# Kernel tuning notes

Measured on AMD Instinct MI355X. Metric: run time of the kernel, lower is better.

## Reference

```python
import jax, jax.numpy as jnp
import numpy as np

ELU = jax.nn.elu
RELU = jax.nn.relu


def _mlp(x, W0, b0, Wh, bh, Wo, bo, act):
    # first hidden layer, stacked middle hidden layers, linear output layer
    h = act(x @ W0 + b0)
    for i in range(Wh.shape[0]):
        h = act(h @ Wh[i] + bh[i])
    return h @ Wo + bo


def _gru_layer(x_seq, h0, Wi, Wh, bi, bh):
    # torch nn.GRU gate math. x_seq: (T,B,I), h0: (B,H)
    xi = x_seq @ Wi.T + bi  # (T,B,3H) precomputed input projection

    def step(h, xt):
        hh = h @ Wh.T + bh
        xr, xz, xn = jnp.split(xt, 3, -1)
        hr, hz, hn = jnp.split(hh, 3, -1)
        r = jax.nn.sigmoid(xr + hr)
        z = jax.nn.sigmoid(xz + hz)
        n = jnp.tanh(xn + r * hn)
        hnew = (1.0 - z) * n + z * h
        return hnew, hnew

    hT, ys = jax.lax.scan(step, h0, xi)
    return ys, hT


def setup_inputs() -> dict:
    key = jax.random.key(0)
    ks = iter(jax.random.split(key, 64))
    B, T = 1024, 512
    S, SE, OE, GH = 4, 16, 16, 16
    OBJ_N, NULL_N, NOBJ = 3, 4, 7
    p = lambda *shape: jax.random.normal(next(ks), shape, jnp.float32) * 0.1
    return dict(
        envs=jax.random.normal(next(ks), (B, 9), jnp.float32),
        states=jax.random.normal(next(ks), (B, T, S), jnp.float32),
        # state embedder: 4 -> [16]*4 -> 16 (relu)
        se_W0=p(S, SE), se_b0=p(SE), se_Wh=p(3, SE, SE), se_bh=p(3, SE), se_Wo=p(SE, SE), se_bo=p(SE),
        # per-object embedders: 3 -> [16]*4 -> 16 (elu), stacked over 3 objects
        oe_W0=p(OBJ_N, 3, OE), oe_b0=p(OBJ_N, OE), oe_Wh=p(OBJ_N, 3, OE, OE), oe_bh=p(OBJ_N, 3, OE),
        oe_Wo=p(OBJ_N, OE, OE), oe_bo=p(OBJ_N, OE),
        null_embed=jax.random.uniform(next(ks), (NULL_N, OE), jnp.float32),
        init_gru_h=jax.random.uniform(next(ks), (2, GH), jnp.float32),
        # attention-score mlp: 32 -> [16]*3 -> 1 (elu)
        att_W0=p(SE + OE, 16), att_b0=p(16), att_Wh=p(2, 16, 16), att_bh=p(2, 16), att_Wo=p(16, 1), att_bo=p(1),
        # GRU: 2 layers, input 128, hidden 16
        gru0_Wi=p(3 * GH, SE + OE * NOBJ), gru0_Wh=p(3 * GH, GH), gru0_bi=p(3 * GH), gru0_bh=p(3 * GH),
        gru1_Wi=p(3 * GH, GH), gru1_Wh=p(3 * GH, GH), gru1_bi=p(3 * GH), gru1_bh=p(3 * GH),
        # relation MLPs: 32 -> [8]*2 -> 8 (elu), stacked over 7 slots
        rel_W0=p(NOBJ, GH + OE, 8), rel_b0=p(NOBJ, 8), rel_Wh=p(NOBJ, 1, 8, 8), rel_bh=p(NOBJ, 1, 8),
        rel_Wo=p(NOBJ, 8, 8), rel_bo=p(NOBJ, 8),
        # final mlp: 72 -> [4]*2 -> 4 (elu)
        fin_W0=p(GH + 8 * NOBJ, S), fin_b0=p(S), fin_Wh=p(1, S, S), fin_bh=p(1, S), fin_Wo=p(S, S), fin_bo=p(S),
        predict_t=0,
    )


def reference(envs, states, se_W0, se_b0, se_Wh, se_bh, se_Wo, se_bo,
              oe_W0, oe_b0, oe_Wh, oe_bh, oe_Wo, oe_bo,
              null_embed, init_gru_h,
              att_W0, att_b0, att_Wh, att_bh, att_Wo, att_bo,
              gru0_Wi, gru0_Wh, gru0_bi, gru0_bh, gru1_Wi, gru1_Wh, gru1_bi, gru1_bh,
              rel_W0, rel_b0, rel_Wh, rel_bh, rel_Wo, rel_bo,
              fin_W0, fin_b0, fin_Wh, fin_bh, fin_Wo, fin_bo,
              predict_t):
    B = envs.shape[0]
    T = states.shape[1]
    NOBJ = rel_W0.shape[0]  # 7 = obj_n + nullobj_n
    OE = null_embed.shape[1]

    # per-object embeddings: split envs into obj_n chunks, run per-slot MLPs (grouped via vmap)
    env_objs = envs.reshape(B, 3, 3).transpose(1, 0, 2)  # (3,B,3)
    obj_real = jax.vmap(lambda x, W0, b0, Wh, bh, Wo, bo: _mlp(x, W0, b0, Wh, bh, Wo, bo, ELU))(
        env_objs, oe_W0, oe_b0, oe_Wh, oe_bh, oe_Wo, oe_bo)  # (3,B,16)
    obj_null = jnp.broadcast_to(null_embed[:, None, :], (null_embed.shape[0], B, OE))  # (4,B,16)
    obj_embd = jnp.concatenate([obj_real, obj_null], 0)           # (7,B,16)
    obj_t = jnp.broadcast_to(obj_embd[:, None], (NOBJ, T, B, OE))  # (7,T,B,16)

    # state embedding over the full sequence (time-major like torch GRU)
    se = _mlp(states.transpose(1, 0, 2), se_W0, se_b0, se_Wh, se_bh, se_Wo, se_bo, RELU)  # (T,B,16)

    # attention scores per object slot
    def score_fn(emb):
        xin = jnp.concatenate([se, emb], -1)  # (T,B,32)
        return _mlp(xin, att_W0, att_b0, att_Wh, att_bh, att_Wo, att_bo, ELU)[..., 0]
    scores = jax.vmap(score_fn)(obj_t)  # (7,T,B)
    # PermuteLayer reverses the slot ordering before softmax over slots
    col_scores = jax.nn.softmax(jnp.flip(scores, 0), axis=0)  # (7,T,B)

    # GRU over [state_emb ; all obj embeds]
    gru_in = jnp.concatenate([se, jnp.moveaxis(obj_t, 0, 2).reshape(T, B, NOBJ * OE)], -1)  # (T,B,128)
    h0 = jnp.broadcast_to(init_gru_h[:, None, :], (2, B, init_gru_h.shape[1]))
    y0, _ = _gru_layer(gru_in, h0[0], gru0_Wi, gru0_Wh, gru0_bi, gru0_bh)
    gru_out, _ = _gru_layer(y0, h0[1], gru1_Wi, gru1_Wh, gru1_bi, gru1_bh)  # (T,B,16)

    # per-slot relation MLPs weighted by attention
    def rel_fn(emb, w, W0, b0, Wh, bh, Wo, bo):
        xin = jnp.concatenate([gru_out, emb], -1)  # (T,B,32)
        r = _mlp(xin, W0, b0, Wh, bh, Wo, bo, ELU)  # (T,B,8)
        return r * w[..., None]
    weighted = jax.vmap(rel_fn)(obj_t, col_scores, rel_W0, rel_b0, rel_Wh, rel_bh, rel_Wo, rel_bo)  # (7,T,B,8)

    final_in = jnp.concatenate([gru_out, jnp.moveaxis(weighted, 0, 2).reshape(T, B, -1)], -1)  # (T,B,72)
    out = _mlp(final_in, fin_W0, fin_b0, fin_Wh, fin_bh, fin_Wo, fin_bo, ELU)  # (T,B,4)
    return out.transpose(1, 0, 2)  # (B,T,4)
```

## Files before the change

kernel.cpp:

```cpp
#include <hip/hip_runtime.h>
#include <hip/hip_bf16.h>
#include <hip/hip_fp16.h>
#include <stdint.h>

#define TLEN 512
#define TCW 48
#define NCHK 11
__device__ __forceinline__ int csize(int i){ return (i == 10) ? 32 : 48; }

typedef unsigned short u16;
typedef unsigned int u32;

__device__ __forceinline__ float b2f(u16 u){ union{u32 i; float f;} v; v.i = ((u32)u)<<16; return v.f; }
__device__ __forceinline__ u16 f2bf(float f){
    union{float f; u32 i;} v; v.f = f;
    u32 b = v.i; b += 0x7fffu + ((b>>16)&1u);
    return (u16)(b>>16);
}
__device__ __forceinline__ float fexp2(float x){ return __builtin_amdgcn_exp2f(x); }
__device__ __forceinline__ float frcp(float x){ return __builtin_amdgcn_rcpf(x); }
#define LOG2E 1.4426950408889634f
__device__ __forceinline__ float elu_f(float x){ return x > 0.f ? x : fexp2(x*LOG2E) - 1.f; }
__device__ __forceinline__ float sigm(float x){ return frcp(1.f + fexp2(-LOG2E*x)); }
__device__ __forceinline__ float tanh_f(float x){ return 1.f - 2.f*frcp(1.f + fexp2((2.f*LOG2E)*x)); }

__device__ __forceinline__ float ldg(const void* p, int i, bool F){
    return F ? ((const float*)p)[i] : b2f(((const u16*)p)[i]);
}

__device__ void fill(float* dst, const void* src, int n, int tid, int nt, bool F){
    for (int i = tid; i < n; i += nt) dst[i] = ldg(src, i, F);
}
__device__ void fillS(float* dst, const void* src, int R, int C, int stride, int tid, int nt, bool F){
    for (int i = tid; i < R*C; i += nt){ int r = i / C, c = i % C; dst[i] = ldg(src, r*stride + c, F); }
}
__device__ void fillT(float* dst, const void* src, int K, int I, int stride, int tid, int nt, bool F){
    for (int idx = tid; idx < K*I; idx += nt){ int i = idx / K, k = idx % K; dst[idx] = ldg(src, k*stride + i, F); }
}

__global__ __launch_bounds__(256,1) void fused(
    const void* envs, const void* states,
    const void* se_W0, const void* se_b0, const void* se_Wh, const void* se_bh, const void* se_Wo, const void* se_bo,
    const void* oe_W0, const void* oe_b0, const void* oe_Wh, const void* oe_bh, const void* oe_Wo, const void* oe_bo,
    const void* null_embed, const void* init_h,
    const void* att_W0, const void* att_b0, const void* att_Wh, const void* att_bh, const void* att_Wo, const void* att_bo,
    const void* gru0_Wi, const void* gru0_Wh, const void* gru0_bi, const void* gru0_bh,
    const void* gru1_Wi, const void* gru1_Wh, const void* gru1_bi, const void* gru1_bh,
    const void* rel_W0, const void* rel_b0, const void* rel_Wh, const void* rel_bh, const void* rel_Wo, const void* rel_bo,
    const void* fin_W0, const void* fin_b0, const void* fin_Wh, const void* fin_bh, const void* fin_Wo, const void* fin_bo,
    void* out)
{
    __shared__ float sW0T[64], sb0[16], sWhT[768], sbh[48], sWoT[256], sbo[16];
    __shared__ float aW0T[256], aWhT[512], abh[32], aWo[16], abo_s[1];
    __shared__ float wi0se[768];
    __shared__ float rW0T[896], rWhT[448], rbh[56], rWoT[448], rbo[56];
    __shared__ float fW0T[288], fb0[4], fWhT[16], fbh[4], fWoT[16], fbo[4];
    __shared__ float E_att[448], E_rel[224], base_xi[192];
    __shared__ float g0bhn[16], g1bi48[48], g1bh48[48];
    __shared__ float uni[14016];
    __shared__ int s_isf32;

    const int tid = threadIdx.x, nt = 256;
    const int blk = blockIdx.x;
    const int wid = tid >> 6, ln = tid & 63;

    _Float16* bufA = (_Float16*)(uni);
    _Float16* bufB = (_Float16*)(uni + 4608);
    _Float16* gruA = (_Float16*)(uni + 9216);
    _Float16* gruB = (_Float16*)(uni + 10752);
    _Float16* cscA = (_Float16*)(uni + 12288);
    _Float16* cscB = (_Float16*)(uni + 12960);
    float*    invA = uni + 13632;
    float*    invB = uni + 13824;

    if (tid == 0){
        const u16* p = (const u16*)se_W0;
        int ok = 1;
        #pragma unroll
        for (int k = 0; k < 8; k++){
            float v = fabsf(b2f(p[2*k]));
            ok &= (v > 1e-12f && v < 16.f) ? 1 : 0;
        }
        s_isf32 = ok ? 0 : 1;
    }
    __syncthreads();
    const bool F = (s_isf32 != 0);

    fillT(sW0T, se_W0, 4, 16, 16, tid, nt, F);
    fill (sb0, se_b0, 16, tid, nt, F);
    for (int l = 0; l < 3; l++) fillT(sWhT + l*256, (const u16*)se_Wh + (F?l*512:l*256), 16, 16, 16, tid, nt, F);
    fill (sbh, se_bh, 48, tid, nt, F);
    fillT(sWoT, se_Wo, 16, 16, 16, tid, nt, F);
    fill (sbo, se_bo, 16, tid, nt, F);
    fillT(aW0T, att_W0, 16, 16, 16, tid, nt, F);
    for (int l = 0; l < 2; l++) fillT(aWhT + l*256, (const u16*)att_Wh + (F?l*512:l*256), 16, 16, 16, tid, nt, F);
    fill (abh, att_bh, 32, tid, nt, F);
    fill (aWo, att_Wo, 16, tid, nt, F);
    fill (abo_s, att_bo, 1, tid, nt, F);
    fillS(wi0se, gru0_Wi, 48, 16, 128, tid, nt, F);
    for (int s = 0; s < 7; s++){
        fillT(rW0T + s*128, (const u16*)rel_W0 + (F?s*512:s*256), 16, 8, 8, tid, nt, F);
        fillT(rWhT + s*64, (const u16*)rel_Wh + (F?s*128:s*64), 8, 8, 8, tid, nt, F);
        fillT(rWoT + s*64, (const u16*)rel_Wo + (F?s*128:s*64), 8, 8, 8, tid, nt, F);
    }
    fill (rbh, rel_bh, 56, tid, nt, F);
    fill (rbo, rel_bo, 56, tid, nt, F);
    fillT(fW0T, fin_W0, 72, 4, 4, tid, nt, F);
    fill (fb0, fin_b0, 4, tid, nt, F);
    fillT(fWhT, fin_Wh, 4, 4, 4, tid, nt, F);
    fill (fbh, fin_bh, 4, tid, nt, F);
    fillT(fWoT, fin_Wo, 4, 4, 4, tid, nt, F);
    fill (fbo, fin_bo, 4, tid, nt, F);
    fill (g0bhn, (const u16*)gru0_bh + (F?64:32), 16, tid, nt, F);
    fill (g1bi48, gru1_bi, 48, tid, nt, F);
    fill (g1bh48, gru1_bh, 48, tid, nt, F);
    float* oeW0T = uni;
    float* oeb0  = uni + 144;
    float* oeWhT = uni + 192;
    float* oebh  = uni + 2496;
    float* oeWoT = uni + 2640;
    float* oebo  = uni + 3408;
    float* aW0To = uni + 3456;
    float* ab0   = uni + 3712;
    float* rW0To = uni + 3728;
    float* objE  = uni + 4624;
    for (int s = 0; s < 3; s++){
        fillT(oeW0T + s*48, (const u16*)oe_W0 + (F?s*96:s*48), 3, 16, 16, tid, nt, F);
        for (int l = 0; l < 3; l++)
            fillT(oeWhT + (s*3+l)*256, (const u16*)oe_Wh + (F?(s*3+l)*512:(s*3+l)*256), 16, 16, 16, tid, nt, F);
        fillT(oeWoT + s*256, (const u16*)oe_Wo + (F?s*512:s*256), 16, 16, 16, tid, nt, F);
    }
    fill(oeb0, oe_b0, 48, tid, nt, F);
    fill(oebh, oe_bh, 144, tid, nt, F);
    fill(oebo, oe_bo, 48, tid, nt, F);
    fillT(aW0To, (const u16*)att_W0 + (F?512:256), 16, 16, 16, tid, nt, F);
    fill (ab0, att_b0, 16, tid, nt, F);
    for (int s = 0; s < 7; s++)
        fillT(rW0To + s*128, (const u16*)rel_W0 + (F?(s*512+256):(s*256+128)), 16, 8, 8, tid, nt, F);
    __syncthreads();

    if (tid < 28){
        int b1 = tid / 7, s = tid % 7;
        float o[16];
        if (s < 3){
            int b = blk*4 + b1;
            float x0 = ldg(envs, b*9+3*s, F), x1 = ldg(envs, b*9+3*s+1, F), x2 = ldg(envs, b*9+3*s+2, F);
            float h[16], h2[16];
            #pragma unroll
            for (int i = 0; i < 16; i++){
                float a = oeb0[s*16+i] + x0*oeW0T[s*48+i*3] + x1*oeW0T[s*48+i*3+1] + x2*oeW0T[s*48+i*3+2];
                h[i] = elu_f(a);
            }
            for (int l = 0; l < 3; l++){
                #pragma unroll
                for (int i = 0; i < 16; i++){
                    float a = oebh[(s*3+l)*16+i];
                    #pragma unroll
                    for (int k = 0; k < 16; k++) a += h[k]*oeWhT[((s*3+l)*16+i)*16+k];
                    h2[i] = elu_f(a);
                }
                #pragma unroll
                for (int i = 0; i < 16; i++) h[i] = h2[i];
            }
            #pragma unroll
            for (int i = 0; i < 16; i++){
                float a = oebo[s*16+i];
                #pragma unroll
                for (int k = 0; k < 16; k++) a += h[k]*oeWoT[(s*16+i)*16+k];
                o[i] = a;
            }
        } else {
            #pragma unroll
            for (int i = 0; i < 16; i++) o[i] = ldg(null_embed, (s-3)*16 + i, F);
        }
        #pragma unroll
        for (int i = 0; i < 16; i++) objE[(b1*7+s)*16 + i] = o[i];
    }
    __syncthreads();

    for (int idx = tid; idx < 448; idx += nt){
        int r = idx % 112, i = r % 16;
        int os = (idx / 16) * 16;
        float a = ab0[i];
        #pragma unroll
        for (int k = 0; k < 16; k++) a += objE[os + k]*aW0To[i*16+k];
        E_att[idx] = a;
    }
    for (int idx = tid; idx < 224; idx += nt){
        int r = idx % 56, s = r / 8, i = r % 8;
        int b1 = idx / 56;
        float a = ldg(rel_b0, s*8+i, F);
        #pragma unroll
        for (int k = 0; k < 16; k++) a += objE[(b1*7+s)*16 + k]*rW0To[(s*8+i)*16+k];
        E_rel[idx] = a;
    }
    for (int idx = tid; idx < 192; idx += nt){
        int b1 = idx / 48, g = idx % 48;
        float a = ldg(gru0_bi, g, F) + (g < 32 ? ldg(gru0_bh, g, F) : 0.f);
        for (int s = 0; s < 7; s++){
            int wb = g*128 + 16 + s*16;
            #pragma unroll
            for (int k = 0; k < 16; k++) a += objE[(b1*7+s)*16 + k]*ldg(gru0_Wi, wb+k, F);
        }
        base_xi[idx] = a;
    }

    const int lj = ln & 15;
    const int gbase = ln & 48;
    float hp0 = 0.f, hp1 = 0.f;
    if (wid == 0){
        hp0 = ldg(init_h, lj, F);
        hp1 = ldg(init_h, 16 + lj, F);
    }
    const int mtid = tid - 64;
    const int b1p = (wid >= 1) ? (mtid / 48) : 0;
    const int tl  = (wid >= 1) ? (mtid % 48) : 0;
    const int bb  = blk*4 + b1p;
    __syncthreads();

    for (int c = 0; c <= NCHK+1; c++){
        if (wid == 0){
            if (c >= 1 && c <= NCHK){
                const int cs = c-1;
                const int tcs = csize(cs);
                const _Float16* xb = (cs&1) ? bufB : bufA;
                _Float16*       gb = (cs&1) ? gruB : gruA;
                float w0r[16], w0z[16], w0n[16], wi1r[16], wi1z[16], wi1n[16], wh1r[16], wh1z[16], wh1n[16];
                #pragma unroll
                for (int k = 0; k < 16; k++){
                    w0r[k]  = ldg(gru0_Wh, lj*16+k, F);
                    w0z[k]  = ldg(gru0_Wh, (16+lj)*16+k, F);
                    w0n[k]  = ldg(gru0_Wh, (32+lj)*16+k, F);
                    wi1r[k] = ldg(gru1_Wi, lj*16+k, F);
                    wi1z[k] = ldg(gru1_Wi, (16+lj)*16+k, F);
                    wi1n[k] = ldg(gru1_Wi, (32+lj)*16+k, F);
                    wh1r[k] = ldg(gru1_Wh, lj*16+k, F);
                    wh1z[k] = ldg(gru1_Wh, (16+lj)*16+k, F);
                    wh1n[k] = ldg(gru1_Wh, (32+lj)*16+k, F);
                }
                const float c0  = g0bhn[lj];
                const float cr  = g1bi48[lj]    + g1bh48[lj];
                const float cz  = g1bi48[16+lj] + g1bh48[16+lj];
                const float can = g1bi48[32+lj];
                const float cbn = g1bh48[32+lj];
                float h0[16], h1[16];
                #pragma unroll
                for (int k = 0; k < 16; k++){ h0[k] = __shfl(hp0, gbase + k); h1[k] = __shfl(hp1, gbase + k); }
                const int grp = ln >> 4;
                int sb = (grp*48 + 0)*48 + lj;
                float xr = (float)xb[sb], xz = (float)xb[sb+16], xn = (float)xb[sb+32];
                for (int s = 0; s < tcs; s++){
                    float xrn = 0.f, xzn = 0.f, xnn2 = 0.f;
                    if (s+1 < tcs){
                        int sb2 = (grp*48 + s+1)*48 + lj;
                        xrn = (float)xb[sb2]; xzn = (float)xb[sb2+16]; xnn2 = (float)xb[sb2+32];
                    }
                    float hr = 0.f, hz = 0.f, hn = c0;
                    #pragma unroll
                    for (int k = 0; k < 16; k++){ hr += h0[k]*w0r[k]; hz += h0[k]*w0z[k]; hn += h0[k]*w0n[k]; }
                    float r = sigm(xr + hr);
                    float z = sigm(xz + hz);
                    float n = tanh_f(xn + r*hn);
                    float h0n = (1.f - z)*n + z*hp0;
                    hp0 = h0n;
                    #pragma unroll
                    for (int k = 0; k < 16; k++) h0[k] = __shfl(h0n, gbase + k);
                    float ar = cr, az = cz, an = can, br = 0.f, bz = 0.f, bn = cbn;
                    #pragma unroll
                    for (int k = 0; k < 16; k++){
                        ar += h0[k]*wi1r[k]; az += h0[k]*wi1z[k]; an += h0[k]*wi1n[k];
                        br += h1[k]*wh1r[k]; bz += h1[k]*wh1z[k]; bn += h1[k]*wh1n[k];
                    }
                    float r1 = sigm(ar + br);
                    float z1 = sigm(az + bz);
                    float n1 = tanh_f(an + r1*bn);
                    float h1n = (1.f - z1)*n1 + z1*hp1;
                    hp1 = h1n;
                    gb[(grp*48 + s)*16 + lj] = (_Float16)h1n;
                    #pragma unroll
                    for (int k = 0; k < 16; k++) h1[k] = __shfl(h1n, gbase + k);
                    xr = xrn; xz = xzn; xn = xnn2;
                }
            }
        } else {
            if (c >= 2){
                const int cp = c-2;
                const int tcp = csize(cp);
                if (tl < tcp){
                    const _Float16* gb = (cp&1) ? gruB : gruA;
                    const _Float16* cb = (cp&1) ? cscB : cscA;
                    const float invv = ((cp&1) ? invB : invA)[b1p*48 + tl];
                    float g[16];
                    #pragma unroll
                    for (int i = 0; i < 16; i++) g[i] = (float)gb[(b1p*48 + tl)*16 + i];
                    float facc[4];
                    #pragma unroll
                    for (int cc = 0; cc < 4; cc++){
                        float a = fb0[cc];
                        #pragma unroll
                        for (int k = 0; k < 16; k++) a += g[k]*fW0T[cc*72+k];
                        facc[cc] = a;
                    }
                    #pragma unroll 1
                    for (int s = 0; s < 7; s++){
                        const float* ep = E_rel + (b1p*7+s)*8;
                        float p1a[8], p2a[8];
                        #pragma unroll
                        for (int i = 0; i < 8; i++){
                            float a = ep[i];
                            #pragma unroll
                            for (int k = 0; k < 16; k++) a += g[k]*rW0T[(s*8+i)*16+k];
                            p1a[i] = elu_f(a);
                        }
                        #pragma unroll
                        for (int i = 0; i < 8; i++){
                            float a = rbh[s*8+i];
                            #pragma unroll
                            for (int k = 0; k < 8; k++) a += p1a[k]*rWhT[(s*8+i)*8+k];
                            p2a[i] = elu_f(a);
                        }
                        float w = (float)cb[(b1p*7+s)*48 + tl] * invv;
                        #pragma unroll
                        for (int i = 0; i < 8; i++){
                            float a = rbo[s*8+i];
                            #pragma unroll
                            for (int k = 0; k < 8; k++) a += p2a[k]*rWoT[(s*8+i)*8+k];
                            float val = a*w;
                            #pragma unroll
                            for (int cc = 0; cc < 4; cc++) facc[cc] += val*fW0T[cc*72+16+s*8+i];
                        }
                    }
                    float f1[4], f2[4], o[4];
                    #pragma unroll
                    for (int cc = 0; cc < 4; cc++) f1[cc] = elu_f(facc[cc]);
                    #pragma unroll
                    for (int cc = 0; cc < 4; cc++){
                        float a = fbh[cc];
                        #pragma unroll
                        for (int k = 0; k < 4; k++) a += f1[k]*fWhT[cc*4+k];
                        f2[cc] = elu_f(a);
                    }
                    #pragma unroll
                    for (int cc = 0; cc < 4; cc++){
                        float a = fbo[cc];
                        #pragma unroll
                        for (int k = 0; k < 4; k++) a += f2[k]*fWoT[cc*4+k];
                        o[cc] = a;
                    }
                    size_t ofs = ((size_t)bb*TLEN + (cp*TCW + tl))*4;
                    if (F){
                        float4 v; v.x = o[0]; v.y = o[1]; v.z = o[2]; v.w = o[3];
                        *(float4*)((float*)out + ofs) = v;
                    } else {
                        u32 lo = (u32)f2bf(o[0]) | ((u32)f2bf(o[1]) << 16);
                        u32 hi = (u32)f2bf(o[2]) | ((u32)f2bf(o[3]) << 16);
                        *(uint2*)((u16*)out + ofs) = make_uint2(lo, hi);
                    }
                }
            }
            if (c < NCHK){
                const int tcc = csize(c);
                if (tl < tcc){
                    _Float16* xb = (c&1) ? bufB : bufA;
                    _Float16* cb = (c&1) ? cscB : cscA;
                    float*   ivb = (c&1) ? invB : invA;
                    const int t = c*TCW + tl;
                    int sbase = ((int)bb*TLEN + t)*4;
                    float x0 = ldg(states, sbase+0, F), x1 = ldg(states, sbase+1, F);
                    float x2 = ldg(states, sbase+2, F), x3 = ldg(states, sbase+3, F);
                    float h[16], h2[16];
                    #pragma unroll
                    for (int i = 0; i < 16; i++){
                        float a = sb0[i] + x0*sW0T[i*4] + x1*sW0T[i*4+1] + x2*sW0T[i*4+2] + x3*sW0T[i*4+3];
                        h[i] = fmaxf(a, 0.f);
                    }
                    for (int l = 0; l < 3; l++){
                        #pragma unroll
                        for (int i = 0; i < 16; i++){
                            float a = sbh[l*16+i];
                            #pragma unroll
                            for (int k = 0; k < 16; k++) a += h[k]*sWhT[(l*16+i)*16+k];
                            h2[i] = fmaxf(a, 0.f);
                        }
                        #pragma unroll
                        for (int i = 0; i < 16; i++) h[i] = h2[i];
                    }
                    float se[16];
                    #pragma unroll
                    for (int i = 0; i < 16; i++){
                        float a = sbo[i];
                        #pragma unroll
                        for (int k = 0; k < 16; k++) a += h[k]*sWoT[i*16+k];
                        se[i] = a;
                    }
                    #pragma unroll 4
                    for (int g = 0; g < 48; g++){
                        float a = base_xi[b1p*48 + g];
                        #pragma unroll
                        for (int k = 0; k < 16; k++) a += se[k]*wi0se[g*16+k];
                        xb[(b1p*48 + tl)*48 + g] = (_Float16)a;
                    }
                    float satt[16];
                    #pragma unroll
                    for (int i = 0; i < 16; i++){
                        float a = 0.f;
                        #pragma unroll
                        for (int k = 0; k < 16; k++) a += se[k]*aW0T[i*16+k];
                        satt[i] = a;
                    }
                    float sum = 0.f;
                    #pragma unroll 1
                    for (int s = 0; s < 7; s++){
                        const float* ep = E_att + (b1p*7+s)*16;
                        float a1[16], a2[16];
                        #pragma unroll
                        for (int i = 0; i < 16; i++) a1[i] = elu_f(satt[i] + ep[i]);
                        #pragma unroll
                        for (int i = 0; i < 16; i++){
                            float a = abh[i];
                            #pragma unroll
                            for (int k = 0; k < 16; k++) a += a1[k]*aWhT[i*16+k];
                            a2[i] = elu_f(a);
                        }
                        #pragma unroll
                        for (int i = 0; i < 16; i++){
                            float a = abh[16+i];
                            #pragma unroll
                            for (int k = 0; k < 16; k++) a += a2[k]*aWhT[256 + i*16+k];
                            a1[i] = elu_f(a);
                        }
                        float a = abo_s[0];
                        #pragma unroll
                        for (int k = 0; k < 16; k++) a += a1[k]*aWo[k];
                        float ex = fexp2(a*LOG2E);
                        cb[(b1p*7+(6-s))*48 + tl] = (_Float16)ex;
                        sum += ex;
                    }
                    ivb[b1p*48 + tl] = frcp(sum);
                }
            }
        }
        __syncthreads();
    }
}

extern "C" void kernel_launch(void* const* d_in, const int* in_sizes, int n_in,
                              void* d_out, int out_size, void* d_ws, size_t ws_size,
                              hipStream_t stream)
{
    (void)in_sizes; (void)n_in; (void)out_size; (void)d_ws; (void)ws_size;
    fused<<<dim3(256), dim3(256), 0, stream>>>(
        d_in[0],  d_in[1],
        d_in[2],  d_in[3],  d_in[4],  d_in[5],  d_in[6],  d_in[7],
        d_in[8],  d_in[9],  d_in[10], d_in[11], d_in[12], d_in[13],
        d_in[14], d_in[15],
        d_in[16], d_in[17], d_in[18], d_in[19], d_in[20], d_in[21],
        d_in[22], d_in[23], d_in[24], d_in[25],
        d_in[26], d_in[27], d_in[28], d_in[29],
        d_in[30], d_in[31], d_in[32], d_in[33], d_in[34], d_in[35],
        d_in[36], d_in[37], d_in[38], d_in[39], d_in[40], d_in[41],
        d_out);
}
```

Measured before the change: 911.7 us.

## Read MLP weights directly from global memory with dtype-templated kernels

Drops most of the shared-memory staging of weights. The state-embedder, attention, relation and final MLPs now load weights straight from global memory through uniform indices, and the loops are reordered so each weight is read once per k. This makes the loads candidates for scalar/constant loads and cuts LDS traffic. The runtime fp32/bf16 check moves into a separate detect kernel, and both template instantiations are launched, with the non-matching one exiting early. The cost is two extra launches and a dependence on the scalar/L1 caches for weight reuse.

```diff
diff --git a/kernel.cpp b/kernel.cpp
--- a/kernel.cpp
+++ b/kernel.cpp
@@ -24,21 +24,36 @@
 __device__ __forceinline__ float sigm(float x){ return frcp(1.f + fexp2(-LOG2E*x)); }
 __device__ __forceinline__ float tanh_f(float x){ return 1.f - 2.f*frcp(1.f + fexp2((2.f*LOG2E)*x)); }
 
-__device__ __forceinline__ float ldg(const void* p, int i, bool F){
-    return F ? ((const float*)p)[i] : b2f(((const u16*)p)[i]);
-}
-
-__device__ void fill(float* dst, const void* src, int n, int tid, int nt, bool F){
-    for (int i = tid; i < n; i += nt) dst[i] = ldg(src, i, F);
-}
-__device__ void fillS(float* dst, const void* src, int R, int C, int stride, int tid, int nt, bool F){
-    for (int i = tid; i < R*C; i += nt){ int r = i / C, c = i % C; dst[i] = ldg(src, r*stride + c, F); }
-}
-__device__ void fillT(float* dst, const void* src, int K, int I, int stride, int tid, int nt, bool F){
-    for (int idx = tid; idx < K*I; idx += nt){ int i = idx / K, k = idx % K; dst[idx] = ldg(src, k*stride + i, F); }
-}
-
+template<bool TF>
+__device__ __forceinline__ float wload(const void* p, int i){
+    if constexpr (TF) return ((const float*)p)[i];
+    else return b2f(((const u16*)p)[i]);
+}
+
+__device__ void fillg(float* dst, const void* src, int n, int tid, int nt, bool F){
+    for (int i = tid; i < n; i += nt) dst[i] = F ? ((const float*)src)[i] : b2f(((const u16*)src)[i]);
+}
+__device__ void fillTg(float* dst, const void* src, int K, int I, int stride, int tid, int nt, bool F){
+    for (int idx = tid; idx < K*I; idx += nt){
+        int i = idx / K, k = idx % K;
+        dst[idx] = F ? ((const float*)src)[k*stride + i] : b2f(((const u16*)src)[k*stride + i]);
+    }
+}
+
+__global__ void detect(const void* se_W0, int* flag){
+    const u16* p = (const u16*)se_W0;
+    int ok = 1;
+    #pragma unroll
+    for (int k = 0; k < 8; k++){
+        float v = fabsf(b2f(p[2*k]));
+        ok &= (v > 1e-12f && v < 16.f) ? 1 : 0;
+    }
+    *flag = ok ? 0 : 1;
+}
+
+template<bool TF>
 __global__ __launch_bounds__(256,1) void fused(
+    const int* flagp,
     const void* envs, const void* states,
     const void* se_W0, const void* se_b0, const void* se_Wh, const void* se_bh, const void* se_Wo, const void* se_bo,
     const void* oe_W0, const void* oe_b0, const void* oe_Wh, const void* oe_bh, const void* oe_Wo, const void* oe_bo,
@@ -50,15 +65,11 @@
     const void* fin_W0, const void* fin_b0, const void* fin_Wh, const void* fin_bh, const void* fin_Wo, const void* fin_bo,
     void* out)
 {
-    __shared__ float sW0T[64], sb0[16], sWhT[768], sbh[48], sWoT[256], sbo[16];
-    __shared__ float aW0T[256], aWhT[512], abh[32], aWo[16], abo_s[1];
-    __shared__ float wi0se[768];
-    __shared__ float rW0T[896], rWhT[448], rbh[56], rWoT[448], rbo[56];
-    __shared__ float fW0T[288], fb0[4], fWhT[16], fbh[4], fWoT[16], fbo[4];
+    if ((*(volatile const int*)flagp != 0) != TF) return;
+
     __shared__ float E_att[448], E_rel[224], base_xi[192];
     __shared__ float g0bhn[16], g1bi48[48], g1bh48[48];
     __shared__ float uni[14016];
-    __shared__ int s_isf32;
 
     const int tid = threadIdx.x, nt = 256;
     const int blk = blockIdx.x;
@@ -73,47 +84,9 @@
     float*    invA = uni + 13632;
     float*    invB = uni + 13824;
 
-    if (tid == 0){
-        const u16* p = (const u16*)se_W0;
-        int ok = 1;
-        #pragma unroll
-        for (int k = 0; k < 8; k++){
-            float v = fabsf(b2f(p[2*k]));
-            ok &= (v > 1e-12f && v < 16.f) ? 1 : 0;
-        }
-        s_isf32 = ok ? 0 : 1;
-    }
-    __syncthreads();
-    const bool F = (s_isf32 != 0);
-
-    fillT(sW0T, se_W0, 4, 16, 16, tid, nt, F);
-    fill (sb0, se_b0, 16, tid, nt, F);
-    for (int l = 0; l < 3; l++) fillT(sWhT + l*256, (const u16*)se_Wh + (F?l*512:l*256), 16, 16, 16, tid, nt, F);
-    fill (sbh, se_bh, 48, tid, nt, F);
-    fillT(sWoT, se_Wo, 16, 16, 16, tid, nt, F);
-    fill (sbo, se_bo, 16, tid, nt, F);
-    fillT(aW0T, att_W0, 16, 16, 16, tid, nt, F);
-    for (int l = 0; l < 2; l++) fillT(aWhT + l*256, (const u16*)att_Wh + (F?l*512:l*256), 16, 16, 16, tid, nt, F);
-    fill (abh, att_bh, 32, tid, nt, F);
-    fill (aWo, att_Wo, 16, tid, nt, F);
-    fill (abo_s, att_bo, 1, tid, nt, F);
-    fillS(wi0se, gru0_Wi, 48, 16, 128, tid, nt, F);
-    for (int s = 0; s < 7; s++){
-        fillT(rW0T + s*128, (const u16*)rel_W0 + (F?s*512:s*256), 16, 8, 8, tid, nt, F);
-        fillT(rWhT + s*64, (const u16*)rel_Wh + (F?s*128:s*64), 8, 8, 8, tid, nt, F);
-        fillT(rWoT + s*64, (const u16*)rel_Wo + (F?s*128:s*64), 8, 8, 8, tid, nt, F);
-    }
-    fill (rbh, rel_bh, 56, tid, nt, F);
-    fill (rbo, rel_bo, 56, tid, nt, F);
-    fillT(fW0T, fin_W0, 72, 4, 4, tid, nt, F);
-    fill (fb0, fin_b0, 4, tid, nt, F);
-    fillT(fWhT, fin_Wh, 4, 4, 4, tid, nt, F);
-    fill (fbh, fin_bh, 4, tid, nt, F);
-    fillT(fWoT, fin_Wo, 4, 4, 4, tid, nt, F);
-    fill (fbo, fin_bo, 4, tid, nt, F);
-    fill (g0bhn, (const u16*)gru0_bh + (F?64:32), 16, tid, nt, F);
-    fill (g1bi48, gru1_bi, 48, tid, nt, F);
-    fill (g1bh48, gru1_bh, 48, tid, nt, F);
+    fillg(g0bhn, (const u16*)gru0_bh + (TF?64:32), 16, tid, nt, TF);
+    fillg(g1bi48, gru1_bi, 48, tid, nt, TF);
+    fillg(g1bh48, gru1_bh, 48, tid, nt, TF);
     float* oeW0T = uni;
     float* oeb0  = uni + 144;
     float* oeWhT = uni + 192;
@@ -125,18 +98,18 @@
     float* rW0To = uni + 3728;
     float* objE  = uni + 4624;
     for (int s = 0; s < 3; s++){
-        fillT(oeW0T + s*48, (const u16*)oe_W0 + (F?s*96:s*48), 3, 16, 16, tid, nt, F);
+        fillTg(oeW0T + s*48, (const u16*)oe_W0 + (TF?s*96:s*48), 3, 16, 16, tid, nt, TF);
         for (int l = 0; l < 3; l++)
-            fillT(oeWhT + (s*3+l)*256, (const u16*)oe_Wh + (F?(s*3+l)*512:(s*3+l)*256), 16, 16, 16, tid, nt, F);
-        fillT(oeWoT + s*256, (const u16*)oe_Wo + (F?s*512:s*256), 16, 16, 16, tid, nt, F);
-    }
-    fill(oeb0, oe_b0, 48, tid, nt, F);
-    fill(oebh, oe_bh, 144, tid, nt, F);
-    fill(oebo, oe_bo, 48, tid, nt, F);
-    fillT(aW0To, (const u16*)att_W0 + (F?512:256), 16, 16, 16, tid, nt, F);
-    fill (ab0, att_b0, 16, tid, nt, F);
+            fillTg(oeWhT + (s*3+l)*256, (const u16*)oe_Wh + (TF?(s*3+l)*512:(s*3+l)*256), 16, 16, 16, tid, nt, TF);
+        fillTg(oeWoT + s*256, (const u16*)oe_Wo + (TF?s*512:s*256), 16, 16, 16, tid, nt, TF);
+    }
+    fillg(oeb0, oe_b0, 48, tid, nt, TF);
+    fillg(oebh, oe_bh, 144, tid, nt, TF);
+    fillg(oebo, oe_bo, 48, tid, nt, TF);
+    fillTg(aW0To, (const u16*)att_W0 + (TF?512:256), 16, 16, 16, tid, nt, TF);
+    fillg(ab0, att_b0, 16, tid, nt, TF);
     for (int s = 0; s < 7; s++)
-        fillT(rW0To + s*128, (const u16*)rel_W0 + (F?(s*512+256):(s*256+128)), 16, 8, 8, tid, nt, F);
+        fillTg(rW0To + s*128, (const u16*)rel_W0 + (TF?(s*512+256):(s*256+128)), 16, 8, 8, tid, nt, TF);
     __syncthreads();
 
     if (tid < 28){
@@ -144,7 +117,7 @@
         float o[16];
         if (s < 3){
             int b = blk*4 + b1;
-            float x0 = ldg(envs, b*9+3*s, F), x1 = ldg(envs, b*9+3*s+1, F), x2 = ldg(envs, b*9+3*s+2, F);
+            float x0 = wload<TF>(envs, b*9+3*s), x1 = wload<TF>(envs, b*9+3*s+1), x2 = wload<TF>(envs, b*9+3*s+2);
             float h[16], h2[16];
             #pragma unroll
             for (int i = 0; i < 16; i++){
@@ -171,7 +144,7 @@
             }
         } else {
             #pragma unroll
-            for (int i = 0; i < 16; i++) o[i] = ldg(null_embed, (s-3)*16 + i, F);
+            for (int i = 0; i < 16; i++) o[i] = wload<TF>(null_embed, (s-3)*16 + i);
         }
         #pragma unroll
         for (int i = 0; i < 16; i++) objE[(b1*7+s)*16 + i] = o[i];
@@ -189,18 +162,18 @@
     for (int idx = tid; idx < 224; idx += nt){
         int r = idx % 56, s = r / 8, i = r % 8;
         int b1 = idx / 56;
-        float a = ldg(rel_b0, s*8+i, F);
+        float a = wload<TF>(rel_b0, s*8+i);
         #pragma unroll
         for (int k = 0; k < 16; k++) a += objE[(b1*7+s)*16 + k]*rW0To[(s*8+i)*16+k];
         E_rel[idx] = a;
     }
     for (int idx = tid; idx < 192; idx += nt){
         int b1 = idx / 48, g = idx % 48;
-        float a = ldg(gru0_bi, g, F) + (g < 32 ? ldg(gru0_bh, g, F) : 0.f);
+        float a = wload<TF>(gru0_bi, g) + (g < 32 ? wload<TF>(gru0_bh, g) : 0.f);
         for (int s = 0; s < 7; s++){
             int wb = g*128 + 16 + s*16;
             #pragma unroll
-            for (int k = 0; k < 16; k++) a += objE[(b1*7+s)*16 + k]*ldg(gru0_Wi, wb+k, F);
+            for (int k = 0; k < 16; k++) a += objE[(b1*7+s)*16 + k]*wload<TF>(gru0_Wi, wb+k);
         }
         base_xi[idx] = a;
     }
@@ -209,8 +182,8 @@
     const int gbase = ln & 48;
     float hp0 = 0.f, hp1 = 0.f;
     if (wid == 0){
-        hp0 = ldg(init_h, lj, F);
-        hp1 = ldg(init_h, 16 + lj, F);
+        hp0 = wload<TF>(init_h, lj);
+        hp1 = wload<TF>(init_h, 16 + lj);
     }
     const int mtid = tid - 64;
     const int b1p = (wid >= 1) ? (mtid / 48) : 0;
@@ -228,15 +201,15 @@
                 float w0r[16], w0z[16], w0n[16], wi1r[16], wi1z[16], wi1n[16], wh1r[16], wh1z[16], wh1n[16];
                 #pragma unroll
                 for (int k = 0; k < 16; k++){
-                    w0r[k]  = ldg(gru0_Wh, lj*16+k, F);
-                    w0z[k]  = ldg(gru0_Wh, (16+lj)*16+k, F);
-                    w0n[k]  = ldg(gru0_Wh, (32+lj)*16+k, F);
-                    wi1r[k] = ldg(gru1_Wi, lj*16+k, F);
-                    wi1z[k] = ldg(gru1_Wi, (16+lj)*16+k, F);
-                    wi1n[k] = ldg(gru1_Wi, (32+lj)*16+k, F);
-                    wh1r[k] = ldg(gru1_Wh, lj*16+k, F);
-                    wh1z[k] = ldg(gru1_Wh, (16+lj)*16+k, F);
-                    wh1n[k] = ldg(gru1_Wh, (32+lj)*16+k, F);
+                    w0r[k]  = wload<TF>(gru0_Wh, lj*16+k);
+                    w0z[k]  = wload<TF>(gru0_Wh, (16+lj)*16+k);
+                    w0n[k]  = wload<TF>(gru0_Wh, (32+lj)*16+k);
+                    wi1r[k] = wload<TF>(gru1_Wi, lj*16+k);
+                    wi1z[k] = wload<TF>(gru1_Wi, (16+lj)*16+k);
+                    wi1n[k] = wload<TF>(gru1_Wi, (32+lj)*16+k);
+                    wh1r[k] = wload<TF>(gru1_Wh, lj*16+k);
+                    wh1z[k] = wload<TF>(gru1_Wh, (16+lj)*16+k);
+                    wh1n[k] = wload<TF>(gru1_Wh, (32+lj)*16+k);
                 }
                 const float c0  = g0bhn[lj];
                 const float cr  = g1bi48[lj]    + g1bh48[lj];
@@ -295,60 +268,77 @@
                     for (int i = 0; i < 16; i++) g[i] = (float)gb[(b1p*48 + tl)*16 + i];
                     float facc[4];
                     #pragma unroll
-                    for (int cc = 0; cc < 4; cc++){
-                        float a = fb0[cc];
-                        #pragma unroll
-                        for (int k = 0; k < 16; k++) a += g[k]*fW0T[cc*72+k];
-                        facc[cc] = a;
+                    for (int cc = 0; cc < 4; cc++) facc[cc] = wload<TF>(fin_b0, cc);
+                    #pragma unroll
+                    for (int k = 0; k < 16; k++){
+                        float gv = g[k];
+                        #pragma unroll
+                        for (int cc = 0; cc < 4; cc++) facc[cc] += gv*wload<TF>(fin_W0, k*4+cc);
                     }
                     #pragma unroll 1
                     for (int s = 0; s < 7; s++){
                         const float* ep = E_rel + (b1p*7+s)*8;
                         float p1a[8], p2a[8];
                         #pragma unroll
+                        for (int i = 0; i < 8; i++) p1a[i] = ep[i];
+                        #pragma unroll
+                        for (int k = 0; k < 16; k++){
+                            float gv = g[k];
+                            #pragma unroll
+                            for (int i = 0; i < 8; i++) p1a[i] += gv*wload<TF>(rel_W0, s*256 + k*8 + i);
+                        }
+                        #pragma unroll
+                        for (int i = 0; i < 8; i++) p1a[i] = elu_f(p1a[i]);
+                        #pragma unroll
+                        for (int i = 0; i < 8; i++) p2a[i] = wload<TF>(rel_bh, s*8+i);
+                        #pragma unroll
+                        for (int k = 0; k < 8; k++){
+                            float pv = p1a[k];
+                            #pragma unroll
+                            for (int i = 0; i < 8; i++) p2a[i] += pv*wload<TF>(rel_Wh, s*64 + k*8 + i);
+                        }
+                        #pragma unroll
+                        for (int i = 0; i < 8; i++) p2a[i] = elu_f(p2a[i]);
+                        float w = (float)cb[(b1p*7+s)*48 + tl] * invv;
+                        float ro[8];
+                        #pragma unroll
+                        for (int i = 0; i < 8; i++) ro[i] = wload<TF>(rel_bo, s*8+i);
+                        #pragma unroll
+                        for (int k = 0; k < 8; k++){
+                            float pv = p2a[k];
+                            #pragma unroll
+                            for (int i = 0; i < 8; i++) ro[i] += pv*wload<TF>(rel_Wo, s*64 + k*8 + i);
+                        }
+                        #pragma unroll
                         for (int i = 0; i < 8; i++){
-                            float a = ep[i];
-                            #pragma unroll
-                            for (int k = 0; k < 16; k++) a += g[k]*rW0T[(s*8+i)*16+k];
-                            p1a[i] = elu_f(a);
-                        }
-                        #pragma unroll
-                        for (int i = 0; i < 8; i++){
-                            float a = rbh[s*8+i];
-                            #pragma unroll
-                            for (int k = 0; k < 8; k++) a += p1a[k]*rWhT[(s*8+i)*8+k];
-                            p2a[i] = elu_f(a);
-                        }
-                        float w = (float)cb[(b1p*7+s)*48 + tl] * invv;
-                        #pragma unroll
-                        for (int i = 0; i < 8; i++){
-                            float a = rbo[s*8+i];
-                            #pragma unroll
-                            for (int k = 0; k < 8; k++) a += p2a[k]*rWoT[(s*8+i)*8+k];
-                            float val = a*w;
-                            #pragma unroll
-                            for (int cc = 0; cc < 4; cc++) facc[cc] += val*fW0T[cc*72+16+s*8+i];
+                            float val = ro[i]*w;
+                            #pragma unroll
+                            for (int cc = 0; cc < 4; cc++) facc[cc] += val*wload<TF>(fin_W0, (16+s*8+i)*4+cc);
                         }
                     }
                     float f1[4], f2[4], o[4];
                     #pragma unroll
                     for (int cc = 0; cc < 4; cc++) f1[cc] = elu_f(facc[cc]);
                     #pragma unroll
-                    for (int cc = 0; cc < 4; cc++){
-                        float a = fbh[cc];
-                        #pragma unroll
-                        for (int k = 0; k < 4; k++) a += f1[k]*fWhT[cc*4+k];
-                        f2[cc] = elu_f(a);
-                    }
-                    #pragma unroll
-                    for (int cc = 0; cc < 4; cc++){
-                        float a = fbo[cc];
-                        #pragma unroll
-                        for (int k = 0; k < 4; k++) a += f2[k]*fWoT[cc*4+k];
-                        o[cc] = a;
+                    for (int cc = 0; cc < 4; cc++) f2[cc] = wload<TF>(fin_bh, cc);
+                    #pragma unroll
+                    for (int k = 0; k < 4; k++){
+                        float fv = f1[k];
+                        #pragma unroll
+                        for (int cc = 0; cc < 4; cc++) f2[cc] += fv*wload<TF>(fin_Wh, k*4+cc);
+                    }
+                    #pragma unroll
+                    for (int cc = 0; cc < 4; cc++) f2[cc] = elu_f(f2[cc]);
+                    #pragma unroll
+                    for (int cc = 0; cc < 4; cc++) o[cc] = wload<TF>(fin_bo, cc);
+                    #pragma unroll
+                    for (int k = 0; k < 4; k++){
+                        float fv = f2[k];
+                        #pragma unroll
+                        for (int cc = 0; cc < 4; cc++) o[cc] += fv*wload<TF>(fin_Wo, k*4+cc);
                     }
                     size_t ofs = ((size_t)bb*TLEN + (cp*TCW + tl))*4;
-                    if (F){
+                    if (TF){
                         float4 v; v.x = o[0]; v.y = o[1]; v.z = o[2]; v.w = o[3];
                         *(float4*)((float*)out + ofs) = v;
                     } else {
@@ -366,47 +356,56 @@
                     float*   ivb = (c&1) ? invB : invA;
                     const int t = c*TCW + tl;
                     int sbase = ((int)bb*TLEN + t)*4;
-                    float x0 = ldg(states, sbase+0, F), x1 = ldg(states, sbase+1, F);
-                    float x2 = ldg(states, sbase+2, F), x3 = ldg(states, sbase+3, F);
+                    float x[4];
+                    #pragma unroll
+                    for (int k = 0; k < 4; k++) x[k] = wload<TF>(states, sbase+k);
                     float h[16], h2[16];
                     #pragma unroll
-                    for (int i = 0; i < 16; i++){
-                        float a = sb0[i] + x0*sW0T[i*4] + x1*sW0T[i*4+1] + x2*sW0T[i*4+2] + x3*sW0T[i*4+3];
-                        h[i] = fmaxf(a, 0.f);
-                    }
+                    for (int i = 0; i < 16; i++) h[i] = wload<TF>(se_b0, i);
+                    #pragma unroll
+                    for (int k = 0; k < 4; k++){
+                        float xv = x[k];
+                        #pragma unroll
+                        for (int i = 0; i < 16; i++) h[i] += xv*wload<TF>(se_W0, k*16+i);
+                    }
+                    #pragma unroll
+                    for (int i = 0; i < 16; i++) h[i] = fmaxf(h[i], 0.f);
                     for (int l = 0; l < 3; l++){
                         #pragma unroll
-                        for (int i = 0; i < 16; i++){
-                            float a = sbh[l*16+i];
-                            #pragma unroll
-                            for (int k = 0; k < 16; k++) a += h[k]*sWhT[(l*16+i)*16+k];
-                            h2[i] = fmaxf(a, 0.f);
-                        }
-                        #pragma unroll
-                        for (int i = 0; i < 16; i++) h[i] = h2[i];
+                        for (int i = 0; i < 16; i++) h2[i] = wload<TF>(se_bh, l*16+i);
+                        #pragma unroll
+                        for (int k = 0; k < 16; k++){
+                            float hv = h[k];
+                            #pragma unroll
+                            for (int i = 0; i < 16; i++) h2[i] += hv*wload<TF>(se_Wh, l*256 + k*16 + i);
+                        }
+                        #pragma unroll
+                        for (int i = 0; i < 16; i++) h[i] = fmaxf(h2[i], 0.f);
                     }
                     float se[16];
                     #pragma unroll
-                    for (int i = 0; i < 16; i++){
-                        float a = sbo[i];
-                        #pragma unroll
-                        for (int k = 0; k < 16; k++) a += h[k]*sWoT[i*16+k];
-                        se[i] = a;
+                    for (int i = 0; i < 16; i++) se[i] = wload<TF>(se_bo, i);
+                    #pragma unroll
+                    for (int k = 0; k < 16; k++){
+                        float hv = h[k];
+                        #pragma unroll
+                        for (int i = 0; i < 16; i++) se[i] += hv*wload<TF>(se_Wo, k*16+i);
                     }
                     #pragma unroll 4
                     for (int g = 0; g < 48; g++){
                         float a = base_xi[b1p*48 + g];
                         #pragma unroll
-                        for (int k = 0; k < 16; k++) a += se[k]*wi0se[g*16+k];
+                        for (int k = 0; k < 16; k++) a += se[k]*wload<TF>(gru0_Wi, g*128 + k);
                         xb[(b1p*48 + tl)*48 + g] = (_Float16)a;
                     }
                     float satt[16];
                     #pragma unroll
-                    for (int i = 0; i < 16; i++){
-                        float a = 0.f;
-                        #pragma unroll
-                        for (int k = 0; k < 16; k++) a += se[k]*aW0T[i*16+k];
-                        satt[i] = a;
+                    for (int i = 0; i < 16; i++) satt[i] = 0.f;
+                    #pragma unroll
+                    for (int k = 0; k < 16; k++){
+                        float sv = se[k];
+                        #pragma unroll
+                        for (int i = 0; i < 16; i++) satt[i] += sv*wload<TF>(att_W0, k*16+i);
                     }
                     float sum = 0.f;
                     #pragma unroll 1
@@ -416,22 +415,26 @@
                         #pragma unroll
                         for (int i = 0; i < 16; i++) a1[i] = elu_f(satt[i] + ep[i]);
                         #pragma unroll
-                        for (int i = 0; i < 16; i++){
-                            float a = abh[i];
-                            #pragma unroll
-                            for (int k = 0; k < 16; k++) a += a1[k]*aWhT[i*16+k];
-                            a2[i] = elu_f(a);
-                        }
-                        #pragma unroll
-                        for (int i = 0; i < 16; i++){
-                            float a = abh[16+i];
-                            #pragma unroll
-                            for (int k = 0; k < 16; k++) a += a2[k]*aWhT[256 + i*16+k];
-                            a1[i] = elu_f(a);
-                        }
-                        float a = abo_s[0];
-                        #pragma unroll
-                        for (int k = 0; k < 16; k++) a += a1[k]*aWo[k];
+                        for (int i = 0; i < 16; i++) a2[i] = wload<TF>(att_bh, i);
+                        #pragma unroll
+                        for (int k = 0; k < 16; k++){
+                            float av = a1[k];
+                            #pragma unroll
+                            for (int i = 0; i < 16; i++) a2[i] += av*wload<TF>(att_Wh, k*16+i);
+                        }
+                        #pragma unroll
+                        for (int i = 0; i < 16; i++) a2[i] = elu_f(a2[i]);
+                        #pragma unroll
+                        for (int i = 0; i < 16; i++) a1[i] = wload<TF>(att_bh, 16+i);
+                        #pragma unroll
+                        for (int k = 0; k < 16; k++){
+                            float av = a2[k];
+                            #pragma unroll
+                            for (int i = 0; i < 16; i++) a1[i] += av*wload<TF>(att_Wh, 256 + k*16+i);
+                        }
+                        float a = wload<TF>(att_bo, 0);
+                        #pragma unroll
+                        for (int k = 0; k < 16; k++) a += elu_f(a1[k])*wload<TF>(att_Wo, k);
                         float ex = fexp2(a*LOG2E);
                         cb[(b1p*7+(6-s))*48 + tl] = (_Float16)ex;
                         sum += ex;
@@ -448,16 +451,16 @@
                               void* d_out, int out_size, void* d_ws, size_t ws_size,
                               hipStream_t stream)
 {
-    (void)in_sizes; (void)n_in; (void)out_size; (void)d_ws; (void)ws_size;
-    fused<<<dim3(256), dim3(256), 0, stream>>>(
-        d_in[0],  d_in[1],
-        d_in[2],  d_in[3],  d_in[4],  d_in[5],  d_in[6],  d_in[7],
-        d_in[8],  d_in[9],  d_in[10], d_in[11], d_in[12], d_in[13],
-        d_in[14], d_in[15],
-        d_in[16], d_in[17], d_in[18], d_in[19], d_in[20], d_in[21],
-        d_in[22], d_in[23], d_in[24], d_in[25],
-        d_in[26], d_in[27], d_in[28], d_in[29],
-        d_in[30], d_in[31], d_in[32], d_in[33], d_in[34], d_in[35],
-        d_in[36], d_in[37], d_in[38], d_in[39], d_in[40], d_in[41],
-        d_out);
-}
+    (void)in_sizes; (void)n_in; (void)out_size; (void)ws_size;
+    int* flag = (int*)d_ws;
+    detect<<<dim3(1), dim3(1), 0, stream>>>(d_in[2], flag);
+#define ARGS flag, d_in[0], d_in[1], d_in[2], d_in[3], d_in[4], d_in[5], d_in[6], d_in[7], \
+    d_in[8], d_in[9], d_in[10], d_in[11], d_in[12], d_in[13], d_in[14], d_in[15], \
+    d_in[16], d_in[17], d_in[18], d_in[19], d_in[20], d_in[21], \
+    d_in[22], d_in[23], d_in[24], d_in[25], d_in[26], d_in[27], d_in[28], d_in[29], \
+    d_in[30], d_in[31], d_in[32], d_in[33], d_in[34], d_in[35], \
+    d_in[36], d_in[37], d_in[38], d_in[39], d_in[40], d_in[41], d_out
+    fused<false><<<dim3(256), dim3(256), 0, stream>>>(ARGS);
+    fused<true><<<dim3(256), dim3(256), 0, stream>>>(ARGS);
+#undef ARGS
+}
```

After: 786.3 us (median of 2 runs). -13.8%, faster.
